# Kernel tuning notes

Measured on AMD Instinct MI355X. Metric: run time of the kernel, lower is better.

## Reference

```python
import jax, jax.numpy as jnp
import numpy as np
from jax import lax

BATCH = 524288
N_LINKS = 8   # body 0 = fixed base, bodies 1..7 have revolute joints
N_DOFS = 7
G = 9.81      # base linear acceleration z-component encodes gravity

def _skew(v):
    x, y, z = v[..., 0], v[..., 1], v[..., 2]
    o = jnp.zeros_like(x)
    return jnp.stack([jnp.stack([o, -z, y], -1),
                      jnp.stack([z, o, -x], -1),
                      jnp.stack([-y, x, o], -1)], -2)

def _rodrigues(axis, theta):
    # rotation about unit axis by theta; broadcasts axis[...,3] with theta[...]
    K = _skew(axis)
    s = jnp.sin(theta)[..., None, None]
    c = jnp.cos(theta)[..., None, None]
    I = jnp.eye(3, dtype=jnp.result_type(theta))
    return I + s * K + (1.0 - c) * (K @ K)

def setup_inputs():
    key = jax.random.key(0)
    ks = jax.random.split(key, 10)
    q = jax.random.normal(ks[0], (BATCH, N_DOFS), jnp.float32)
    qd = jax.random.normal(ks[1], (BATCH, N_DOFS), jnp.float32)
    qdd_des = jax.random.normal(ks[2], (BATCH, N_DOFS), jnp.float32)
    # fixed (URDF) joint transforms: valid random rotations + link-offset translations
    ax = jax.random.normal(ks[3], (N_LINKS, 3), jnp.float32)
    ax = ax / jnp.linalg.norm(ax, axis=-1, keepdims=True)
    ang = jax.random.uniform(ks[4], (N_LINKS,), jnp.float32, -1.0, 1.0)
    rot_fix = _rodrigues(ax, ang)
    trans_fix = jax.random.uniform(ks[5], (N_LINKS, 3), jnp.float32, -0.25, 0.25)
    # single-coordinate joint axes with signs, as in URDF revolute joints
    joint_axes = jnp.asarray([[0, 0, 1], [0, 1, 0], [0, 0, 1], [0, -1, 0],
                              [0, 0, 1], [0, 1, 0], [0, 0, 1]], jnp.float32)
    mass = jax.random.uniform(ks[6], (N_LINKS,), jnp.float32, 0.5, 4.0)
    com = 0.05 * jax.random.normal(ks[7], (N_LINKS, 3), jnp.float32)
    A = 0.1 * jax.random.normal(ks[8], (N_LINKS, 3, 3), jnp.float32)
    inertia = A @ jnp.swapaxes(A, -1, -2) + 0.05 * jnp.eye(3, dtype=jnp.float32)
    damping = jax.random.uniform(ks[9], (N_DOFS,), jnp.float32, 0.01, 0.2)
    return dict(q=q, qd=qd, qdd_des=qdd_des, rot_fix=rot_fix, trans_fix=trans_fix,
                joint_axes=joint_axes, mass=mass, com=com, inertia=inertia, damping=damping)

def reference(q, qd, qdd_des, rot_fix, trans_fix, joint_axes, mass, com, inertia, damping):
    # Batched recursive Newton-Euler inverse dynamics over a serial chain,
    # matching DifferentiableRobotModel.compute_inverse_dynamics (gravity+damping on).
    B, D = q.shape
    # joint pose of body i(=dof j+1): rotation = rot_fix[i] @ R(axis_j, q_j), translation = trans_fix[i]
    Rq = _rodrigues(joint_axes[None, :, :], q)                     # [B,D,3,3]
    R = jnp.einsum('dij,bdjk->dbik', rot_fix[1:], Rq)              # [D,B,3,3]
    p = trans_fix[1:]                                              # [D,3]
    jv = qd.T[:, :, None] * joint_axes[:, None, :]                 # [D,B,3] joint angular vel
    ja = qdd_des.T[:, :, None] * joint_axes[:, None, :]            # [D,B,3] joint angular acc

    z = jnp.zeros((B, 3), q.dtype)
    base_acc_lin = z.at[:, 2].set(G)

    # forward pass: propagate spatial velocity/acceleration root -> leaf
    def fwd_step(carry, xs):
        vl, va, al, aa = carry
        Ri, pi, jvi, jai = xs
        Rt = jnp.swapaxes(Ri, -1, -2)
        pinv = -jnp.einsum('bij,j->bi', Rt, pi)
        # SpatialMotionVec.transform with inverse joint pose (Rt, pinv)
        va_n = jnp.einsum('bij,bj->bi', Rt, va)
        vl_n = jnp.einsum('bij,bj->bi', Rt, vl) + jnp.cross(pinv, va_n)
        va_i = va_n + jvi
        vl_i = vl_n
        aa_n = jnp.einsum('bij,bj->bi', Rt, aa)
        al_n = jnp.einsum('bij,bj->bi', Rt, al) + jnp.cross(pinv, aa_n)
        # acc = parent_acc(transformed) + joint_acc + vel x joint_vel (joint_vel.lin = 0)
        aa_i = aa_n + jai + jnp.cross(va_i, jvi)
        al_i = al_n + jnp.cross(vl_i, jvi)
        new = (vl_i, va_i, al_i, aa_i)
        return new, new

    _, (vl, va, al, aa) = lax.scan(fwd_step, (z, z, base_acc_lin, z), (R, p, jv, ja))

    # spatial inertia (about body frame origin) acting on motion vectors
    m = mass[1:, None, None]                                       # [D,1,1]
    mc = mass[1:, None] * com[1:]                                  # [D,3]
    cs = _skew(com[1:])
    Io = inertia[1:] + mass[1:, None, None] * (cs @ jnp.swapaxes(cs, -1, -2))

    def imul(lin, ang):
        return (m * lin + jnp.cross(ang, mc[:, None, :]),
                jnp.einsum('dij,dbj->dbi', Io, ang) + jnp.cross(mc[:, None, :], lin))

    Ia_l, Ia_a = imul(al, aa)
    Iv_l, Iv_a = imul(vl, va)
    # f = I*acc + vel x* (I*vel)
    f_l = Ia_l + jnp.cross(va, Iv_l)
    f_a = Ia_a + jnp.cross(va, Iv_a) + jnp.cross(vl, Iv_l)

    # backward pass: accumulate forces leaf -> root; tau_j = f.ang . axis_j
    def bwd_step(carry, xs):
        cl, ca = carry
        fl, fa, Ri, pi, axi = xs
        tl = fl + cl
        ta = fa + ca
        tau = jnp.einsum('bi,i->b', ta, axi)
        # SpatialForceVec.transform with joint pose (Ri, pi)
        nl = jnp.einsum('bij,bj->bi', Ri, tl)
        na = jnp.einsum('bij,bj->bi', Ri, ta) + jnp.cross(pi[None, :], nl)
        return (nl, na), tau

    _, taus = lax.scan(bwd_step, (z, z), (f_l, f_a, R, p, joint_axes), reverse=True)
    return jnp.swapaxes(taus, 0, 1) + damping[None, :] * qd        # [B,D]
```

## Files before the change

kernel.cpp:

```cpp
#include <hip/hip_runtime.h>

#define NDOF 7
#define NPARK 5
#define BLK 128
#define RPB 256
#define CST_STRIDE 24
#define CST_TOT (NDOF * CST_STRIDE)
#define SF_V2 (NPARK * 6 * BLK)

typedef float f32x2 __attribute__((ext_vector_type(2)));

__device__ __forceinline__ f32x2 splat(float v) { f32x2 r; r.x = v; r.y = v; return r; }

struct PV3 { f32x2 x, y, z; };
__device__ __forceinline__ PV3 operator+(PV3 a, PV3 b) { return {a.x + b.x, a.y + b.y, a.z + b.z}; }
__device__ __forceinline__ PV3 operator-(PV3 a, PV3 b) { return {a.x - b.x, a.y - b.y, a.z - b.z}; }
__device__ __forceinline__ PV3 operator*(f32x2 s, PV3 a) { return {s * a.x, s * a.y, s * a.z}; }
__device__ __forceinline__ PV3 cross(PV3 a, PV3 b) {
    return {a.y * b.z - a.z * b.y, a.z * b.x - a.x * b.z, a.x * b.y - a.y * b.x};
}
__device__ __forceinline__ f32x2 dot(PV3 a, PV3 b) { return a.x * b.x + a.y * b.y + a.z * b.z; }
__device__ __forceinline__ PV3 uv(float x, float y, float z) { return {splat(x), splat(y), splat(z)}; }

__global__ void rnea_prep(const float* __restrict__ rot_fix,
                          const float* __restrict__ trans_fix,
                          const float* __restrict__ mass_g,
                          const float* __restrict__ com_g,
                          const float* __restrict__ inertia_g,
                          const float* __restrict__ damping_g,
                          float* __restrict__ cst) {
    const int d = threadIdx.x;
    if (d >= NDOF) return;
    float* o = cst + d * CST_STRIDE;
    const float* F = rot_fix + (1 + d) * 9;
#pragma unroll
    for (int j = 0; j < 3; j++)
#pragma unroll
        for (int i = 0; i < 3; i++) o[j * 3 + i] = F[i * 3 + j];
#pragma unroll
    for (int i = 0; i < 3; i++) o[9 + i] = trans_fix[(1 + d) * 3 + i];
    const float m = mass_g[1 + d];
    const float c0 = com_g[(1 + d) * 3 + 0];
    const float c1 = com_g[(1 + d) * 3 + 1];
    const float c2 = com_g[(1 + d) * 3 + 2];
    const float* I = inertia_g + (1 + d) * 9;
    o[12] = I[0] + m * (c1 * c1 + c2 * c2);
    o[13] = I[1] - m * c0 * c1;
    o[14] = I[2] - m * c0 * c2;
    o[15] = I[4] + m * (c0 * c0 + c2 * c2);
    o[16] = I[5] - m * c1 * c2;
    o[17] = I[8] + m * (c0 * c0 + c1 * c1);
    o[18] = m;
    o[19] = m * c0;
    o[20] = m * c1;
    o[21] = m * c2;
    o[22] = damping_g[d];
    o[23] = 0.f;
}

template <int AX>
__device__ __forceinline__ void make_R(PV3 Fc0, PV3 Fc1, PV3 Fc2, f32x2 s, f32x2 c,
                                       PV3& R0, PV3& R1, PV3& R2) {
    if (AX == 0) {
        R0 = c * Fc0 + s * Fc1;
        R1 = c * Fc1 - s * Fc0;
        R2 = Fc2;
    } else if (AX == 1) {
        R0 = c * Fc0 - s * Fc2;
        R1 = Fc1;
        R2 = s * Fc0 + c * Fc2;
    } else {
        R0 = c * Fc0 + s * Fc2;
        R1 = Fc1;
        R2 = c * Fc2 - s * Fc0;
    }
}

template <int AX>
__device__ __forceinline__ void fwd_step(float4 A0, float4 A1, float4 A2, float4 A3,
                                         float4 A4, float4 A5, f32x2 s, f32x2 c,
                                         f32x2 qd, f32x2 qdd, PV3& vl, PV3& va, PV3& al,
                                         PV3& aa, PV3& fl, PV3& fa) {
    const PV3 Fc0 = uv(A0.x, A0.y, A0.z);
    const PV3 Fc1 = uv(A0.w, A1.x, A1.y);
    const PV3 Fc2 = uv(A1.z, A1.w, A2.x);
    const PV3 p = uv(A2.y, A2.z, A2.w);
    const f32x2 I00 = splat(A3.x), I01 = splat(A3.y), I02 = splat(A3.z);
    const f32x2 I11 = splat(A3.w), I12 = splat(A4.x), I22 = splat(A4.y);
    const f32x2 m = splat(A4.z);
    const PV3 mc = uv(A4.w, A5.x, A5.y);

    PV3 R0, R1, R2;
    make_R<AX>(Fc0, Fc1, Fc2, s, c, R0, R1, R2);

    PV3 w1 = vl + cross(va, p);
    PV3 w2 = al + cross(aa, p);
    PV3 nvl{dot(R0, w1), dot(R1, w1), dot(R2, w1)};
    PV3 nva{dot(R0, va), dot(R1, va), dot(R2, va)};
    PV3 nal{dot(R0, w2), dot(R1, w2), dot(R2, w2)};
    PV3 naa{dot(R0, aa), dot(R1, aa), dot(R2, aa)};

    if (AX == 0) {
        va = {nva.x, nva.y, nva.z + qd};
        aa = {naa.x + va.y * qd, naa.y - va.x * qd, naa.z + qdd};
        vl = nvl;
        al = {nal.x + vl.y * qd, nal.y - vl.x * qd, nal.z};
    } else if (AX == 1) {
        va = {nva.x, nva.y + qd, nva.z};
        aa = {naa.x - va.z * qd, naa.y + qdd, naa.z + va.x * qd};
        vl = nvl;
        al = {nal.x - vl.z * qd, nal.y, nal.z + vl.x * qd};
    } else {
        va = {nva.x, nva.y - qd, nva.z};
        aa = {naa.x + va.z * qd, naa.y - qdd, naa.z - va.x * qd};
        vl = nvl;
        al = {nal.x + vl.z * qd, nal.y, nal.z - vl.x * qd};
    }

    PV3 Ial = m * al + cross(aa, mc);
    PV3 Iaa = PV3{I00 * aa.x + I01 * aa.y + I02 * aa.z,
                  I01 * aa.x + I11 * aa.y + I12 * aa.z,
                  I02 * aa.x + I12 * aa.y + I22 * aa.z} + cross(mc, al);
    PV3 Ivl = m * vl + cross(va, mc);
    PV3 Iva = PV3{I00 * va.x + I01 * va.y + I02 * va.z,
                  I01 * va.x + I11 * va.y + I12 * va.z,
                  I02 * va.x + I12 * va.y + I22 * va.z} + cross(mc, vl);
    fl = Ial + cross(va, Ivl);
    fa = Iaa + cross(va, Iva) + cross(vl, Ivl);
}

template <int AX>
__device__ __forceinline__ f32x2 bwd_core(float4 A0, float4 A1, float4 A2,
                                          f32x2 s, f32x2 c,
                                          PV3 fl, PV3 fa, PV3& cl, PV3& ca) {
    const PV3 Fc0 = uv(A0.x, A0.y, A0.z);
    const PV3 Fc1 = uv(A0.w, A1.x, A1.y);
    const PV3 Fc2 = uv(A1.z, A1.w, A2.x);
    const PV3 p = uv(A2.y, A2.z, A2.w);

    PV3 tl = fl + cl;
    PV3 ta = fa + ca;
    f32x2 tau;
    if (AX == 0) tau = ta.z;
    else if (AX == 1) tau = ta.y;
    else tau = splat(0.f) - ta.y;

    PV3 R0, R1, R2;
    make_R<AX>(Fc0, Fc1, Fc2, s, c, R0, R1, R2);
    PV3 nl = tl.x * R0 + tl.y * R1 + tl.z * R2;
    PV3 na = ta.x * R0 + ta.y * R1 + ta.z * R2 + cross(p, nl);
    cl = nl;
    ca = na;
    return tau;
}

__device__ __forceinline__ int axid(int d) { return (d & 1) ? ((d == 3) ? 2 : 1) : 0; }

__global__ __launch_bounds__(BLK) void rnea_main(
    const float* __restrict__ q_g, const float* __restrict__ qd_g,
    const float* __restrict__ qdd_g, const float* __restrict__ cst,
    float* __restrict__ out, int nbatch) {
    __shared__ __align__(16) float sC[CST_TOT];
    __shared__ f32x2 sF[SF_V2];
    const int t = threadIdx.x;
    const int rowA = blockIdx.x * RPB + t;
    const int rowB = rowA + BLK;
    const bool okA = rowA < nbatch;
    const bool okB = rowB < nbatch;
    const int rcA = okA ? rowA : (nbatch - 1);
    const int rcB = okB ? rowB : (nbatch - 1);
    const size_t goA = (size_t)rcA * NDOF;
    const size_t goB = (size_t)rcB * NDOF;

    if (t < CST_TOT / 4)
        reinterpret_cast<float4*>(sC)[t] = reinterpret_cast<const float4*>(cst)[t];
    __syncthreads();

    PV3 vl{splat(0.f), splat(0.f), splat(0.f)};
    PV3 va = vl, aa = vl;
    PV3 al{splat(0.f), splat(0.f), splat(9.81f)};
    f32x2 qn, qdn, qddn;
    qn.x = q_g[goA];   qn.y = q_g[goB];
    qdn.x = qd_g[goA]; qdn.y = qd_g[goB];
    qddn.x = qdd_g[goA]; qddn.y = qdd_g[goB];
#pragma clang loop unroll(disable)
    for (int d = 0; d < NPARK; ++d) {
        const f32x2 q = qn, qd = qdn, qdd = qddn;
        qn.x = q_g[goA + d + 1];   qn.y = q_g[goB + d + 1];
        qdn.x = qd_g[goA + d + 1]; qdn.y = qd_g[goB + d + 1];
        qddn.x = qdd_g[goA + d + 1]; qddn.y = qdd_g[goB + d + 1];
        f32x2 s, c;
        s.x = __sinf(q.x); s.y = __sinf(q.y);
        c.x = __cosf(q.x); c.y = __cosf(q.y);
        const float4* C4 = reinterpret_cast<const float4*>(sC) + d * 6;
        const float4 A0 = C4[0], A1 = C4[1], A2 = C4[2], A3 = C4[3], A4 = C4[4], A5 = C4[5];
        PV3 fl, fa;
        switch (axid(d)) {
            case 0: fwd_step<0>(A0, A1, A2, A3, A4, A5, s, c, qd, qdd, vl, va, al, aa, fl, fa); break;
            case 1: fwd_step<1>(A0, A1, A2, A3, A4, A5, s, c, qd, qdd, vl, va, al, aa, fl, fa); break;
            default: fwd_step<2>(A0, A1, A2, A3, A4, A5, s, c, qd, qdd, vl, va, al, aa, fl, fa); break;
        }
        f32x2* r = sF + d * 6 * BLK + t;
        r[0 * BLK] = fl.x; r[1 * BLK] = fl.y; r[2 * BLK] = fl.z;
        r[3 * BLK] = fa.x; r[4 * BLK] = fa.y; r[5 * BLK] = fa.z;
    }

    const f32x2 q5 = qn, qd5 = qdn, qdd5 = qddn;
    f32x2 q6, qd6, qdd6;
    q6.x = q_g[goA + 6];   q6.y = q_g[goB + 6];
    qd6.x = qd_g[goA + 6]; qd6.y = qd_g[goB + 6];
    qdd6.x = qdd_g[goA + 6]; qdd6.y = qdd_g[goB + 6];
    f32x2 s5, c5, s6, c6;
    s5.x = __sinf(q5.x); s5.y = __sinf(q5.y);
    c5.x = __cosf(q5.x); c5.y = __cosf(q5.y);
    s6.x = __sinf(q6.x); s6.y = __sinf(q6.y);
    c6.x = __cosf(q6.x); c6.y = __cosf(q6.y);
    PV3 cl{splat(0.f), splat(0.f), splat(0.f)}, ca = cl;
    f32x2 tau5, tau6;
    {
        const float4* C5 = reinterpret_cast<const float4*>(sC) + 5 * 6;
        const float4 B0 = C5[0], B1 = C5[1], B2 = C5[2], B3 = C5[3], B4 = C5[4], B5 = C5[5];
        const float4* C6 = reinterpret_cast<const float4*>(sC) + 6 * 6;
        const float4 D0 = C6[0], D1 = C6[1], D2 = C6[2], D3 = C6[3], D4 = C6[4], D5 = C6[5];
        PV3 fl5, fa5, fl6, fa6;
        fwd_step<1>(B0, B1, B2, B3, B4, B5, s5, c5, qd5, qdd5, vl, va, al, aa, fl5, fa5);
        fwd_step<0>(D0, D1, D2, D3, D4, D5, s6, c6, qd6, qdd6, vl, va, al, aa, fl6, fa6);
        tau6 = bwd_core<0>(D0, D1, D2, s6, c6, fl6, fa6, cl, ca) + splat(D5.z) * qd6;
        tau5 = bwd_core<1>(B0, B1, B2, s5, c5, fl5, fa5, cl, ca) + splat(B5.z) * qd5;
    }

#pragma clang loop unroll(disable)
    for (int d = NPARK - 1; d >= 0; --d) {
        f32x2 q, qd;
        q.x = q_g[goA + d];  q.y = q_g[goB + d];
        qd.x = qd_g[goA + d]; qd.y = qd_g[goB + d];
        f32x2 s, c;
        s.x = __sinf(q.x); s.y = __sinf(q.y);
        c.x = __cosf(q.x); c.y = __cosf(q.y);
        const float4* C4 = reinterpret_cast<const float4*>(sC) + d * 6;
        const float4 A0 = C4[0], A1 = C4[1], A2 = C4[2];
        const float damp = sC[d * CST_STRIDE + 22];
        f32x2* r = sF + d * 6 * BLK + t;
        const PV3 fl{r[0 * BLK], r[1 * BLK], r[2 * BLK]};
        const PV3 fa{r[3 * BLK], r[4 * BLK], r[5 * BLK]};
        f32x2 tau;
        switch (axid(d)) {
            case 0: tau = bwd_core<0>(A0, A1, A2, s, c, fl, fa, cl, ca); break;
            case 1: tau = bwd_core<1>(A0, A1, A2, s, c, fl, fa, cl, ca); break;
            default: tau = bwd_core<2>(A0, A1, A2, s, c, fl, fa, cl, ca); break;
        }
        r[0] = tau + splat(damp) * qd;
    }

    if (okA) {
#pragma unroll
        for (int d = 0; d < NPARK; ++d) out[goA + d] = sF[d * 6 * BLK + t].x;
        out[goA + 5] = tau5.x;
        out[goA + 6] = tau6.x;
    }
    if (okB) {
#pragma unroll
        for (int d = 0; d < NPARK; ++d) out[goB + d] = sF[d * 6 * BLK + t].y;
        out[goB + 5] = tau5.y;
        out[goB + 6] = tau6.y;
    }
}

extern "C" void kernel_launch(void* const* d_in, const int* in_sizes, int n_in,
                              void* d_out, int out_size, void* d_ws, size_t ws_size,
                              hipStream_t stream) {
    const float* q = (const float*)d_in[0];
    const float* qd = (const float*)d_in[1];
    const float* qdd = (const float*)d_in[2];
    const float* rot_fix = (const float*)d_in[3];
    const float* trans_fix = (const float*)d_in[4];
    const float* mass = (const float*)d_in[6];
    const float* com = (const float*)d_in[7];
    const float* inertia = (const float*)d_in[8];
    const float* damping = (const float*)d_in[9];
    float* out = (float*)d_out;
    float* cst = (float*)d_ws;

    const int n_elem = in_sizes[0];
    const int B = n_elem / NDOF;
    const int grid = (B + RPB - 1) / RPB;

    rnea_prep<<<1, 64, 0, stream>>>(rot_fix, trans_fix, mass, com, inertia, damping, cst);
    rnea_main<<<grid, BLK, 0, stream>>>(q, qd, qdd, cst, out, B);
}
```

Before: 118.9 us.

## Fuse constant prep into main kernel and cache sin/cos in LDS for backward pass

Removes the separate single-block prep kernel launch: each block now has its first 7 threads compute the per-link constants directly into shared memory. The forward loop also stores each link's sin/cos pair in shared memory, so the backward loop no longer reloads q from global memory or recomputes the trig functions. The trade-offs are that every block redoes the small constant computation with scattered global reads before the barrier, and the shared-memory scratch grows from 6 to 8 slots per link, which may reduce occupancy.

```diff
diff --git a/kernel.cpp b/kernel.cpp
--- a/kernel.cpp
+++ b/kernel.cpp
@@ -6,7 +6,8 @@
 #define RPB 256
 #define CST_STRIDE 24
 #define CST_TOT (NDOF * CST_STRIDE)
-#define SF_V2 (NPARK * 6 * BLK)
+#define SLOTS 8
+#define SF_V2 (NPARK * SLOTS * BLK)
 
 typedef float f32x2 __attribute__((ext_vector_type(2)));
 
@@ -21,42 +22,6 @@
 }
 __device__ __forceinline__ f32x2 dot(PV3 a, PV3 b) { return a.x * b.x + a.y * b.y + a.z * b.z; }
 __device__ __forceinline__ PV3 uv(float x, float y, float z) { return {splat(x), splat(y), splat(z)}; }
-
-__global__ void rnea_prep(const float* __restrict__ rot_fix,
-                          const float* __restrict__ trans_fix,
-                          const float* __restrict__ mass_g,
-                          const float* __restrict__ com_g,
-                          const float* __restrict__ inertia_g,
-                          const float* __restrict__ damping_g,
-                          float* __restrict__ cst) {
-    const int d = threadIdx.x;
-    if (d >= NDOF) return;
-    float* o = cst + d * CST_STRIDE;
-    const float* F = rot_fix + (1 + d) * 9;
-#pragma unroll
-    for (int j = 0; j < 3; j++)
-#pragma unroll
-        for (int i = 0; i < 3; i++) o[j * 3 + i] = F[i * 3 + j];
-#pragma unroll
-    for (int i = 0; i < 3; i++) o[9 + i] = trans_fix[(1 + d) * 3 + i];
-    const float m = mass_g[1 + d];
-    const float c0 = com_g[(1 + d) * 3 + 0];
-    const float c1 = com_g[(1 + d) * 3 + 1];
-    const float c2 = com_g[(1 + d) * 3 + 2];
-    const float* I = inertia_g + (1 + d) * 9;
-    o[12] = I[0] + m * (c1 * c1 + c2 * c2);
-    o[13] = I[1] - m * c0 * c1;
-    o[14] = I[2] - m * c0 * c2;
-    o[15] = I[4] + m * (c0 * c0 + c2 * c2);
-    o[16] = I[5] - m * c1 * c2;
-    o[17] = I[8] + m * (c0 * c0 + c1 * c1);
-    o[18] = m;
-    o[19] = m * c0;
-    o[20] = m * c1;
-    o[21] = m * c2;
-    o[22] = damping_g[d];
-    o[23] = 0.f;
-}
 
 template <int AX>
 __device__ __forceinline__ void make_R(PV3 Fc0, PV3 Fc1, PV3 Fc2, f32x2 s, f32x2 c,
@@ -158,7 +123,10 @@
 
 __global__ __launch_bounds__(BLK) void rnea_main(
     const float* __restrict__ q_g, const float* __restrict__ qd_g,
-    const float* __restrict__ qdd_g, const float* __restrict__ cst,
+    const float* __restrict__ qdd_g,
+    const float* __restrict__ rot_fix, const float* __restrict__ trans_fix,
+    const float* __restrict__ mass_g, const float* __restrict__ com_g,
+    const float* __restrict__ inertia_g, const float* __restrict__ damping_g,
     float* __restrict__ out, int nbatch) {
     __shared__ __align__(16) float sC[CST_TOT];
     __shared__ f32x2 sF[SF_V2];
@@ -172,8 +140,34 @@
     const size_t goA = (size_t)rcA * NDOF;
     const size_t goB = (size_t)rcB * NDOF;
 
-    if (t < CST_TOT / 4)
-        reinterpret_cast<float4*>(sC)[t] = reinterpret_cast<const float4*>(cst)[t];
+    if (t < NDOF) {
+        const int d = t;
+        float* o = sC + d * CST_STRIDE;
+        const float* F = rot_fix + (1 + d) * 9;
+#pragma unroll
+        for (int j = 0; j < 3; j++)
+#pragma unroll
+            for (int i = 0; i < 3; i++) o[j * 3 + i] = F[i * 3 + j];
+#pragma unroll
+        for (int i = 0; i < 3; i++) o[9 + i] = trans_fix[(1 + d) * 3 + i];
+        const float m = mass_g[1 + d];
+        const float c0 = com_g[(1 + d) * 3 + 0];
+        const float c1 = com_g[(1 + d) * 3 + 1];
+        const float c2 = com_g[(1 + d) * 3 + 2];
+        const float* I = inertia_g + (1 + d) * 9;
+        o[12] = I[0] + m * (c1 * c1 + c2 * c2);
+        o[13] = I[1] - m * c0 * c1;
+        o[14] = I[2] - m * c0 * c2;
+        o[15] = I[4] + m * (c0 * c0 + c2 * c2);
+        o[16] = I[5] - m * c1 * c2;
+        o[17] = I[8] + m * (c0 * c0 + c1 * c1);
+        o[18] = m;
+        o[19] = m * c0;
+        o[20] = m * c1;
+        o[21] = m * c2;
+        o[22] = damping_g[d];
+        o[23] = 0.f;
+    }
     __syncthreads();
 
     PV3 vl{splat(0.f), splat(0.f), splat(0.f)};
@@ -200,9 +194,10 @@
             case 1: fwd_step<1>(A0, A1, A2, A3, A4, A5, s, c, qd, qdd, vl, va, al, aa, fl, fa); break;
             default: fwd_step<2>(A0, A1, A2, A3, A4, A5, s, c, qd, qdd, vl, va, al, aa, fl, fa); break;
         }
-        f32x2* r = sF + d * 6 * BLK + t;
+        f32x2* r = sF + d * SLOTS * BLK + t;
         r[0 * BLK] = fl.x; r[1 * BLK] = fl.y; r[2 * BLK] = fl.z;
         r[3 * BLK] = fa.x; r[4 * BLK] = fa.y; r[5 * BLK] = fa.z;
+        r[6 * BLK] = s;    r[7 * BLK] = c;
     }
 
     const f32x2 q5 = qn, qd5 = qdn, qdd5 = qddn;
@@ -231,18 +226,16 @@
 
 #pragma clang loop unroll(disable)
     for (int d = NPARK - 1; d >= 0; --d) {
-        f32x2 q, qd;
-        q.x = q_g[goA + d];  q.y = q_g[goB + d];
+        f32x2 qd;
         qd.x = qd_g[goA + d]; qd.y = qd_g[goB + d];
-        f32x2 s, c;
-        s.x = __sinf(q.x); s.y = __sinf(q.y);
-        c.x = __cosf(q.x); c.y = __cosf(q.y);
         const float4* C4 = reinterpret_cast<const float4*>(sC) + d * 6;
         const float4 A0 = C4[0], A1 = C4[1], A2 = C4[2];
         const float damp = sC[d * CST_STRIDE + 22];
-        f32x2* r = sF + d * 6 * BLK + t;
+        f32x2* r = sF + d * SLOTS * BLK + t;
         const PV3 fl{r[0 * BLK], r[1 * BLK], r[2 * BLK]};
         const PV3 fa{r[3 * BLK], r[4 * BLK], r[5 * BLK]};
+        const f32x2 s = r[6 * BLK];
+        const f32x2 c = r[7 * BLK];
         f32x2 tau;
         switch (axid(d)) {
             case 0: tau = bwd_core<0>(A0, A1, A2, s, c, fl, fa, cl, ca); break;
@@ -254,13 +247,13 @@
 
     if (okA) {
 #pragma unroll
-        for (int d = 0; d < NPARK; ++d) out[goA + d] = sF[d * 6 * BLK + t].x;
+        for (int d = 0; d < NPARK; ++d) out[goA + d] = sF[d * SLOTS * BLK + t].x;
         out[goA + 5] = tau5.x;
         out[goA + 6] = tau6.x;
     }
     if (okB) {
 #pragma unroll
-        for (int d = 0; d < NPARK; ++d) out[goB + d] = sF[d * 6 * BLK + t].y;
+        for (int d = 0; d < NPARK; ++d) out[goB + d] = sF[d * SLOTS * BLK + t].y;
         out[goB + 5] = tau5.y;
         out[goB + 6] = tau6.y;
     }
@@ -279,12 +272,11 @@
     const float* inertia = (const float*)d_in[8];
     const float* damping = (const float*)d_in[9];
     float* out = (float*)d_out;
-    float* cst = (float*)d_ws;
 
     const int n_elem = in_sizes[0];
     const int B = n_elem / NDOF;
     const int grid = (B + RPB - 1) / RPB;
 
-    rnea_prep<<<1, 64, 0, stream>>>(rot_fix, trans_fix, mass, com, inertia, damping, cst);
-    rnea_main<<<grid, BLK, 0, stream>>>(q, qd, qdd, cst, out, B);
-}
+    rnea_main<<<grid, BLK, 0, stream>>>(q, qd, qdd, rot_fix, trans_fix, mass, com,
+                                        inertia, damping, out, B);
+}
```

New measurement: 120.8 us. Within noise of the previous version (+1.6%).
